# Performance work log

Hardware: AMD Instinct MI355X
Metric: run time of the kernel (lower is better)

## Reference

```python
import jax, jax.numpy as jnp
import numpy as np

NUM_NODES = 50000
FEAT_DIM = 256
CLIPS = 8
DIM = 128
K_NEIGH = 32
B, S = 2048, 10


def setup_inputs() -> dict:
    key = jax.random.key(0)
    k1, k2, k3, k4 = jax.random.split(key, 4)
    nodes = jax.random.randint(k1, (B, S), 0, NUM_NODES, dtype=jnp.int64)
    adj = jax.random.randint(k2, (NUM_NODES, K_NEIGH), 0, NUM_NODES, dtype=jnp.int64)
    features = jax.random.normal(k3, (NUM_NODES, FEAT_DIM), dtype=jnp.float32)
    # xavier-uniform-ish scale for local_weight [clips, dim, feat_dim]
    limit = float(np.sqrt(6.0 / (DIM + FEAT_DIM)))
    local_weight = jax.random.uniform(k4, (CLIPS, DIM, FEAT_DIM), dtype=jnp.float32,
                                      minval=-limit, maxval=limit)
    return {"nodes": nodes, "adj": adj, "features": features, "local_weight": local_weight}


def reference(nodes, adj, features, local_weight):
    # order == 1: one hop of mean aggregation over sampled neighbor lists
    nodes_flat = nodes.reshape(-1)                      # [n]
    neigh = adj[nodes_flat]                             # [n, K] irregular gather
    feat = features[neigh].mean(axis=1)                 # [n, d] gather + mean
    # einsum('ckd,dn->ckn').permute(2,0,1) == einsum('ckd,nd->nck')
    local_out = jnp.einsum('ckd,nd->nck', local_weight, feat)   # [n, clips, dim]
    local_embs = jax.nn.relu(local_out)
    return local_embs.reshape(nodes.shape[0], nodes.shape[1], local_weight.shape[0], -1)
```

## Files before the change

kernel.cpp:

```cpp
#include <hip/hip_runtime.h>

#define FEAT_DIM 256
#define K_NEIGH  32
#define NROWS    20480
#define NOUT     1024
#define NUM_NODES 50000

typedef __attribute__((ext_vector_type(8))) short bf16x8;
typedef __attribute__((ext_vector_type(4))) float f32x4;

__device__ __forceinline__ unsigned short f2bf(float f) {
    unsigned int u = __builtin_bit_cast(unsigned int, f);
    u += 0x7fffu + ((u >> 16) & 1u);
    return (unsigned short)(u >> 16);
}
__device__ __forceinline__ float bf2f(unsigned short h) {
    unsigned int u = ((unsigned int)h) << 16;
    return __builtin_bit_cast(float, u);
}
__device__ __forceinline__ void gload16(const void* g, void* l) {
    __builtin_amdgcn_global_load_lds(
        (const __attribute__((address_space(1))) unsigned int*)g,
        (__attribute__((address_space(3))) unsigned int*)l, 16, 0, 0);
}

__global__ __launch_bounds__(256) void wcvt_kernel(const float* __restrict__ w,
                                                   unsigned short* __restrict__ wb) {
    int i = (blockIdx.x * 256 + threadIdx.x) * 4;
    float4 v = *(const float4*)(w + i);
    ushort4 o;
    o.x = f2bf(v.x); o.y = f2bf(v.y); o.z = f2bf(v.z); o.w = f2bf(v.w);
    *(ushort4*)(wb + i) = o;
}

__global__ __launch_bounds__(256) void fcvt_kernel(const float* __restrict__ f,
                                                   unsigned short* __restrict__ fb) {
    long i = (long)(blockIdx.x * 256 + threadIdx.x) * 8;
    float4 v0 = *(const float4*)(f + i);
    float4 v1 = *(const float4*)(f + i + 4);
    ushort4 o0, o1;
    o0.x = f2bf(v0.x); o0.y = f2bf(v0.y); o0.z = f2bf(v0.z); o0.w = f2bf(v0.w);
    o1.x = f2bf(v1.x); o1.y = f2bf(v1.y); o1.z = f2bf(v1.z); o1.w = f2bf(v1.w);
    *(ushort4*)(fb + i) = o0;
    *(ushort4*)(fb + i + 4) = o1;
}

__global__ __launch_bounds__(256) void agg_bf_kernel(const int* __restrict__ nodes,
                                                     const int* __restrict__ adj,
                                                     const unsigned short* __restrict__ fb,
                                                     unsigned short* __restrict__ feat) {
    int half = threadIdx.x >> 7;
    int t = threadIdx.x & 127;
    int row = blockIdx.x * 2 + half;
    int node = nodes[row];
    const int* arow = adj + (long)node * K_NEIGH;
    float a0 = 0.f, a1 = 0.f;
    #pragma unroll
    for (int k = 0; k < K_NEIGH; ++k) {
        long nb = arow[k];
        unsigned int v = *(const unsigned int*)(fb + nb * FEAT_DIM + 2 * t);
        a0 += bf2f((unsigned short)(v & 0xffffu));
        a1 += bf2f((unsigned short)(v >> 16));
    }
    ushort2 o;
    o.x = f2bf(a0 * (1.0f / K_NEIGH));
    o.y = f2bf(a1 * (1.0f / K_NEIGH));
    *(ushort2*)(feat + (long)row * FEAT_DIM + 2 * t) = o;
}

__global__ __launch_bounds__(256) void agg_f32_kernel(const int* __restrict__ nodes,
                                                      const int* __restrict__ adj,
                                                      const float* __restrict__ features,
                                                      unsigned short* __restrict__ feat) {
    int row = blockIdx.x;
    int t = threadIdx.x;
    int node = nodes[row];
    const int* arow = adj + (long)node * K_NEIGH;
    float acc = 0.f;
    #pragma unroll
    for (int k = 0; k < K_NEIGH; ++k) {
        long nb = arow[k];
        acc += features[nb * FEAT_DIM + t];
    }
    feat[(long)row * FEAT_DIM + t] = f2bf(acc * (1.0f / K_NEIGH));
}

__global__ __launch_bounds__(256) void gemm_kernel(const unsigned short* __restrict__ A,
                                                   const unsigned short* __restrict__ Bw,
                                                   float* __restrict__ C) {
    __shared__ short As[128 * 32];
    __shared__ short Bs[128 * 32];

    int t = threadIdx.x;
    int wave = t >> 6, lane = t & 63;
    int wm = wave >> 1, wn = wave & 1;
    int m0 = blockIdx.x * 128, n0 = blockIdx.y * 128;
    int lr = lane & 15;
    int lk = (lane >> 4) * 8;

    int srow = t >> 2;
    int sseg = (t & 3) * 8;
    const short* Ag = (const short*)A + (long)(m0 + srow) * FEAT_DIM + sseg;
    const short* Bg = (const short*)Bw + (long)(n0 + srow) * FEAT_DIM + sseg;
    short* Al = As + t * 8;
    short* Bl = Bs + t * 8;

    f32x4 acc[4][4] = {};

    for (int kb = 0; kb < FEAT_DIM; kb += 32) {
        if (kb) __syncthreads();
        gload16(Ag + kb, Al);
        gload16(Ag + 64 * FEAT_DIM + kb, Al + 64 * 32);
        gload16(Bg + kb, Bl);
        gload16(Bg + 64 * FEAT_DIM + kb, Bl + 64 * 32);
        __syncthreads();

        bf16x8 a[4], b[4];
        #pragma unroll
        for (int i = 0; i < 4; ++i)
            a[i] = *(const bf16x8*)(As + (wm * 64 + i * 16 + lr) * 32 + lk);
        #pragma unroll
        for (int j = 0; j < 4; ++j)
            b[j] = *(const bf16x8*)(Bs + (wn * 64 + j * 16 + lr) * 32 + lk);
        #pragma unroll
        for (int i = 0; i < 4; ++i)
            #pragma unroll
            for (int j = 0; j < 4; ++j)
                acc[i][j] = __builtin_amdgcn_mfma_f32_16x16x32_bf16(a[i], b[j], acc[i][j], 0, 0, 0);
    }

    int crow0 = m0 + wm * 64 + (lane >> 4) * 4;
    int ccol0 = n0 + wn * 64 + lr;
    #pragma unroll
    for (int i = 0; i < 4; ++i)
        #pragma unroll
        for (int j = 0; j < 4; ++j)
            #pragma unroll
            for (int r = 0; r < 4; ++r) {
                float v = acc[i][j][r];
                C[(long)(crow0 + i * 16 + r) * NOUT + ccol0 + j * 16] = v > 0.f ? v : 0.f;
            }
}

extern "C" void kernel_launch(void* const* d_in, const int* in_sizes, int n_in,
                              void* d_out, int out_size, void* d_ws, size_t ws_size,
                              hipStream_t stream) {
    const int*   nodes    = (const int*)d_in[0];
    const int*   adj      = (const int*)d_in[1];
    const float* features = (const float*)d_in[2];
    const float* lw       = (const float*)d_in[3];
    float*       out      = (float*)d_out;

    const size_t fbf_elems  = (size_t)NUM_NODES * FEAT_DIM;
    const size_t feat_elems = (size_t)NROWS * FEAT_DIM;
    const size_t need = (fbf_elems + feat_elems + (size_t)NOUT * FEAT_DIM) * 2;

    if (ws_size >= need) {
        unsigned short* fbf  = (unsigned short*)d_ws;
        unsigned short* feat = fbf + fbf_elems;
        unsigned short* wb   = feat + feat_elems;

        wcvt_kernel<<<(NOUT * FEAT_DIM) / (256 * 4), 256, 0, stream>>>(lw, wb);
        fcvt_kernel<<<(int)(fbf_elems / (256 * 8)), 256, 0, stream>>>(features, fbf);
        agg_bf_kernel<<<NROWS / 2, 256, 0, stream>>>(nodes, adj, fbf, feat);
        gemm_kernel<<<dim3(NROWS / 128, NOUT / 128), 256, 0, stream>>>(feat, wb, out);
    } else {
        unsigned short* feat = (unsigned short*)d_ws;
        unsigned short* wb   = feat + feat_elems;

        wcvt_kernel<<<(NOUT * FEAT_DIM) / (256 * 4), 256, 0, stream>>>(lw, wb);
        agg_f32_kernel<<<NROWS, 256, 0, stream>>>(nodes, adj, features, feat);
        gemm_kernel<<<dim3(NROWS / 128, NOUT / 128), 256, 0, stream>>>(feat, wb, out);
    }
}
```

Before: 86.97 us.

## Slice bf16 feature table by dimension and aggregate per slice for cache locality

The bf16 feature copy is rewritten in a sliced layout of 8 slices of 32 dims, each slice contiguous across all nodes. The aggregation kernel now processes one slice per block, with 4 threads per row each loading 16-byte vectors and the neighbor indices loaded as int4. The aim is for the gather working set per slice (about 3.2MB) to stay in cache, and to use wider loads instead of 4-byte per-thread gathers. In exchange, each row's neighbor list is read 8 times, and every 64-byte gather touches a separate cache line.

```diff
diff --git a/kernel.cpp b/kernel.cpp
--- a/kernel.cpp
+++ b/kernel.cpp
@@ -5,6 +5,8 @@
 #define NROWS    20480
 #define NOUT     1024
 #define NUM_NODES 50000
+#define SLICE_DIM 32
+#define NSLICE    8
 
 typedef __attribute__((ext_vector_type(8))) short bf16x8;
 typedef __attribute__((ext_vector_type(4))) float f32x4;
@@ -33,39 +35,52 @@
     *(ushort4*)(wb + i) = o;
 }
 
-__global__ __launch_bounds__(256) void fcvt_kernel(const float* __restrict__ f,
+__global__ __launch_bounds__(256) void fcvt_sliced(const float* __restrict__ f,
                                                    unsigned short* __restrict__ fb) {
-    long i = (long)(blockIdx.x * 256 + threadIdx.x) * 8;
-    float4 v0 = *(const float4*)(f + i);
-    float4 v1 = *(const float4*)(f + i + 4);
-    ushort4 o0, o1;
-    o0.x = f2bf(v0.x); o0.y = f2bf(v0.y); o0.z = f2bf(v0.z); o0.w = f2bf(v0.w);
-    o1.x = f2bf(v1.x); o1.y = f2bf(v1.y); o1.z = f2bf(v1.z); o1.w = f2bf(v1.w);
-    *(ushort4*)(fb + i) = o0;
-    *(ushort4*)(fb + i + 4) = o1;
+    int t = threadIdx.x;
+    int node = blockIdx.x * 16 + (t >> 4);
+    int part = t & 15;
+    int slice = part >> 1, half = part & 1;
+    const float* src = f + (long)node * FEAT_DIM + part * 16;
+    unsigned short o[16];
+    #pragma unroll
+    for (int j = 0; j < 16; j += 4) {
+        float4 v = *(const float4*)(src + j);
+        o[j] = f2bf(v.x); o[j+1] = f2bf(v.y); o[j+2] = f2bf(v.z); o[j+3] = f2bf(v.w);
+    }
+    unsigned short* dst = fb + ((long)slice * NUM_NODES + node) * SLICE_DIM + half * 16;
+    *(bf16x8*)dst = *(const bf16x8*)o;
+    *(bf16x8*)(dst + 8) = *(const bf16x8*)(o + 8);
 }
 
-__global__ __launch_bounds__(256) void agg_bf_kernel(const int* __restrict__ nodes,
-                                                     const int* __restrict__ adj,
-                                                     const unsigned short* __restrict__ fb,
-                                                     unsigned short* __restrict__ feat) {
-    int half = threadIdx.x >> 7;
-    int t = threadIdx.x & 127;
-    int row = blockIdx.x * 2 + half;
+__global__ __launch_bounds__(256) void agg_sliced(const int* __restrict__ nodes,
+                                                  const int* __restrict__ adj,
+                                                  const unsigned short* __restrict__ fb,
+                                                  unsigned short* __restrict__ feat) {
+    int slice = blockIdx.x & 7;
+    int chunk = blockIdx.x >> 3;
+    int t = threadIdx.x;
+    int row = chunk * 64 + (t >> 2);
+    int d8 = (t & 3) * 8;
     int node = nodes[row];
     const int* arow = adj + (long)node * K_NEIGH;
-    float a0 = 0.f, a1 = 0.f;
+    int nbr[K_NEIGH];
+    #pragma unroll
+    for (int kk = 0; kk < K_NEIGH / 4; ++kk)
+        *(int4*)(nbr + kk * 4) = ((const int4*)arow)[kk];
+
+    const unsigned short* base = fb + (long)slice * NUM_NODES * SLICE_DIM + d8;
+    float acc[8] = {};
     #pragma unroll
     for (int k = 0; k < K_NEIGH; ++k) {
-        long nb = arow[k];
-        unsigned int v = *(const unsigned int*)(fb + nb * FEAT_DIM + 2 * t);
-        a0 += bf2f((unsigned short)(v & 0xffffu));
-        a1 += bf2f((unsigned short)(v >> 16));
+        bf16x8 v = *(const bf16x8*)(base + (long)nbr[k] * SLICE_DIM);
+        #pragma unroll
+        for (int j = 0; j < 8; ++j) acc[j] += bf2f((unsigned short)v[j]);
     }
-    ushort2 o;
-    o.x = f2bf(a0 * (1.0f / K_NEIGH));
-    o.y = f2bf(a1 * (1.0f / K_NEIGH));
-    *(ushort2*)(feat + (long)row * FEAT_DIM + 2 * t) = o;
+    unsigned short o[8];
+    #pragma unroll
+    for (int j = 0; j < 8; ++j) o[j] = f2bf(acc[j] * (1.0f / K_NEIGH));
+    *(bf16x8*)(feat + (long)row * FEAT_DIM + slice * SLICE_DIM + d8) = *(const bf16x8*)o;
 }
 
 __global__ __launch_bounds__(256) void agg_f32_kernel(const int* __restrict__ nodes,
@@ -161,8 +176,8 @@
         unsigned short* wb   = feat + feat_elems;
 
         wcvt_kernel<<<(NOUT * FEAT_DIM) / (256 * 4), 256, 0, stream>>>(lw, wb);
-        fcvt_kernel<<<(int)(fbf_elems / (256 * 8)), 256, 0, stream>>>(features, fbf);
-        agg_bf_kernel<<<NROWS / 2, 256, 0, stream>>>(nodes, adj, fbf, feat);
+        fcvt_sliced<<<NUM_NODES / 16, 256, 0, stream>>>(features, fbf);
+        agg_sliced<<<(NROWS / 64) * NSLICE, 256, 0, stream>>>(nodes, adj, fbf, feat);
         gemm_kernel<<<dim3(NROWS / 128, NOUT / 128), 256, 0, stream>>>(feat, wb, out);
     } else {
         unsigned short* feat = (unsigned short*)d_ws;
```

Measured after the change: 78.27 us. -10.0%, faster.
